# Kernel optimization log

Measured on AMD Instinct MI355X. Metric: run time of the kernel, lower is better.

The kernel has to match this reference:

```python
import jax, jax.numpy as jnp
import numpy as np

D_MODEL = 1024
NHEADS = 16
DIM_K = D_MODEL // NHEADS


def setup_inputs() -> dict:
    key = jax.random.key(0)
    ks = jax.random.split(key, 7)
    B, S = 4, 2048
    scale = 1.0 / np.sqrt(D_MODEL)
    return {
        "Q": jax.random.normal(ks[0], (B, S, D_MODEL), jnp.float32),
        "K": jax.random.normal(ks[1], (B, S, D_MODEL), jnp.float32),
        "V": jax.random.normal(ks[2], (B, S, D_MODEL), jnp.float32),
        "Wq": jax.random.normal(ks[3], (D_MODEL, D_MODEL), jnp.float32) * scale,
        "Wk": jax.random.normal(ks[4], (D_MODEL, D_MODEL), jnp.float32) * scale,
        "Wv": jax.random.normal(ks[5], (D_MODEL, D_MODEL), jnp.float32) * scale,
        "Wo": jax.random.normal(ks[6], (D_MODEL, D_MODEL), jnp.float32) * scale,
    }


def _split(x):
    # [B,S,D] -> [B,H,S,dk]
    B, S, _ = x.shape
    return x.reshape(B, S, NHEADS, DIM_K).transpose(0, 2, 1, 3)


def reference(Q, K, V, Wq, Wk, Wv, Wo):
    # nn.Linear(x) = x @ W.T; weights stored torch-style [out, in]
    q = _split(Q @ Wq.T)  # [B,H,S,dk]
    k = _split(K @ Wk.T)
    v = _split(V @ Wv.T)
    scores = jnp.einsum("bhsd,bhtd->bhst", q, k) / jnp.sqrt(jnp.float32(DIM_K))
    attn = jax.nn.softmax(scores, axis=-1)
    out = jnp.einsum("bhst,bhtd->bhsd", attn, v)  # [B,H,S,dk]
    B, H, S, dk = out.shape
    out = out.transpose(0, 2, 1, 3).reshape(B, S, H * dk)
    return out @ Wo.T
```

## Files before the change

kernel.cpp:

```cpp
#include <hip/hip_runtime.h>
#include <math.h>
#include <stdint.h>

#define D_MODEL 1024
#define NHEADS  16
#define DK      64
#define BATCH   4
#define SEQ     2048
#define MROWS   (BATCH * SEQ)
#define TENS    ((size_t)MROWS * D_MODEL)
#define WELT    ((size_t)D_MODEL * D_MODEL)

typedef __attribute__((ext_vector_type(8))) _Float16 f16x8;
typedef __attribute__((ext_vector_type(2))) __fp16 h16x2;
typedef __attribute__((ext_vector_type(4))) float f32x4;
typedef __attribute__((ext_vector_type(8))) unsigned short us8;
typedef __attribute__((ext_vector_type(4))) unsigned short us4;

__device__ __forceinline__ unsigned short f2h(float x) {
    _Float16 h = (_Float16)x;
    return __builtin_bit_cast(unsigned short, h);
}

#if __has_builtin(__builtin_amdgcn_exp2f)
__device__ __forceinline__ float fexp2(float x) { return __builtin_amdgcn_exp2f(x); }
#else
__device__ __forceinline__ float fexp2(float x) { return exp2f(x); }
#endif

__device__ __forceinline__ void gld_lds16(const void* g, void* l) {
    __builtin_amdgcn_global_load_lds(
        (__attribute__((address_space(1))) void*)(uintptr_t)(g),
        (__attribute__((address_space(3))) void*)(unsigned)(uintptr_t)(l),
        16, 0, 0);
}

__global__ __launch_bounds__(256)
void convert_kernel(const float* __restrict__ q, const float* __restrict__ k,
                    const float* __restrict__ v, const float* __restrict__ wq,
                    const float* __restrict__ wk, const float* __restrict__ wv,
                    const float* __restrict__ wo, unsigned short* __restrict__ dst)
{
    const int seg = blockIdx.y;
    const float* src;
    size_t n, doff;
    if (seg < 3) {
        src = (seg == 0) ? q : (seg == 1) ? k : v;
        n = TENS; doff = (size_t)seg * TENS;
    } else {
        src = (seg == 3) ? wq : (seg == 4) ? wk : (seg == 5) ? wv : wo;
        n = WELT; doff = 3 * TENS + (size_t)(seg - 3) * WELT;
    }
    size_t i = ((size_t)blockIdx.x * 256 + threadIdx.x) * 4;
    if (i >= n) return;
    float4 f = *(const float4*)(src + i);
    us4 o = { f2h(f.x), f2h(f.y), f2h(f.z), f2h(f.w) };
    *(us4*)(dst + doff + i) = o;
}

__device__ __forceinline__
void gemm_body(const unsigned short* __restrict__ A,
               const unsigned short* __restrict__ B,
               void* __restrict__ C, int N, int K, int omode,
               unsigned short* As, unsigned short* Bs)
{
    const int tid  = threadIdx.x;
    const int wave = tid >> 6;
    const int lane = tid & 63;
    const int g    = lane >> 4;
    const int m15  = lane & 15;
    const int bm   = blockIdx.x * 128;
    const int bn   = blockIdx.y * 128;

    const int srw = lane >> 3;
    const int lc  = (lane & 7) ^ srw;

    const int wr = (wave >> 1) * 64;
    const int wc = (wave & 1) * 64;

    f32x4 acc[4][4];
#pragma unroll
    for (int i = 0; i < 4; ++i)
#pragma unroll
        for (int j = 0; j < 4; ++j) acc[i][j] = (f32x4){0.f, 0.f, 0.f, 0.f};

    for (int k0 = 0; k0 < K; k0 += 64) {
        __syncthreads();
#pragma unroll
        for (int i = 0; i < 4; ++i) {
            const int rb = wave * 32 + i * 8;
            gld_lds16(A + (size_t)(bm + rb + srw) * K + k0 + lc * 8,
                      &As[rb * 64]);
            gld_lds16(B + (size_t)(bn + rb + srw) * K + k0 + lc * 8,
                      &Bs[rb * 64]);
        }
        __syncthreads();

#pragma unroll
        for (int t = 0; t < 2; ++t) {
            f16x8 af[4], bf[4];
#pragma unroll
            for (int i = 0; i < 4; ++i) {
                int row = wr + i * 16 + m15;
                int pc  = (4 * t + g) ^ (row & 7);
                af[i] = *(const f16x8*)&As[row * 64 + pc * 8];
            }
#pragma unroll
            for (int j = 0; j < 4; ++j) {
                int row = wc + j * 16 + m15;
                int pc  = (4 * t + g) ^ (row & 7);
                bf[j] = *(const f16x8*)&Bs[row * 64 + pc * 8];
            }
#pragma unroll
            for (int i = 0; i < 4; ++i)
#pragma unroll
                for (int j = 0; j < 4; ++j)
                    acc[i][j] = __builtin_amdgcn_mfma_f32_16x16x32_f16(
                        af[i], bf[j], acc[i][j], 0, 0, 0);
        }
    }

#pragma unroll
    for (int i = 0; i < 4; ++i) {
        const int gm0 = bm + wr + i * 16 + g * 4;
#pragma unroll
        for (int j = 0; j < 4; ++j) {
            const int gn = bn + wc + j * 16 + m15;
            if (omode == 0) {
#pragma unroll
                for (int r = 0; r < 4; ++r)
                    ((float*)C)[(size_t)(gm0 + r) * N + gn] = acc[i][j][r];
            } else if (omode == 1) {
#pragma unroll
                for (int r = 0; r < 4; ++r)
                    ((unsigned short*)C)[(size_t)(gm0 + r) * N + gn] = f2h(acc[i][j][r]);
            } else {
                const int b_ = gm0 >> 11, s_ = gm0 & 2047;
                const int h_ = gn >> 6,  d_ = gn & 63;
                us4 o = { f2h(acc[i][j][0]), f2h(acc[i][j][1]),
                          f2h(acc[i][j][2]), f2h(acc[i][j][3]) };
                *(us4*)((unsigned short*)C +
                        (((size_t)(b_ * NHEADS + h_) * DK + d_) << 11) + s_) = o;
            }
        }
    }
}

__global__ __launch_bounds__(256)
void proj3_kernel(const unsigned short* __restrict__ qb,
                  const unsigned short* __restrict__ kb,
                  const unsigned short* __restrict__ vb,
                  const unsigned short* __restrict__ wq,
                  const unsigned short* __restrict__ wk,
                  const unsigned short* __restrict__ wv,
                  unsigned short* __restrict__ qproj,
                  unsigned short* __restrict__ kproj,
                  unsigned short* __restrict__ vtw)
{
    __shared__ unsigned short As[128 * 64];
    __shared__ unsigned short Bs[128 * 64];
    const int z = blockIdx.z;
    const unsigned short* A = (z == 0) ? qb : (z == 1) ? kb : vb;
    const unsigned short* B = (z == 0) ? wq : (z == 1) ? wk : wv;
    void* C = (z == 0) ? (void*)qproj : (z == 1) ? (void*)kproj : (void*)vtw;
    gemm_body(A, B, C, D_MODEL, D_MODEL, (z == 2) ? 2 : 1, As, Bs);
}

__global__ __launch_bounds__(256)
void gemm_out_kernel(const unsigned short* __restrict__ A,
                     const unsigned short* __restrict__ B,
                     float* __restrict__ C)
{
    __shared__ unsigned short As[128 * 64];
    __shared__ unsigned short Bs[128 * 64];
    gemm_body(A, B, C, D_MODEL, D_MODEL, 0, As, Bs);
}

__global__ __launch_bounds__(256, 2)
void attn_kernel(const unsigned short* __restrict__ qp,
                 const unsigned short* __restrict__ kp,
                 const unsigned short* __restrict__ vt,
                 unsigned short* __restrict__ ao)
{
    __shared__ unsigned short Ks[64 * 64];
    __shared__ unsigned short VTs[64 * 64];
    __shared__ unsigned short Ps[4][64 * 72];

    const int tid = threadIdx.x;
    const int w = tid >> 6, lane = tid & 63;
    const int g = lane >> 4, m15 = lane & 15;
    const int qt = blockIdx.x, h = blockIdx.y, b = blockIdx.z;

    const int q0 = qt * 256 + w * 64;
    const size_t rowbase = (size_t)b * SEQ;

    const int srw = lane >> 3;
    const int lc  = (lane & 7) ^ srw;

    const _Float16 qscale = (_Float16)(0.125f * 1.4426950408889634f);
    f16x8 qf[4][2];
#pragma unroll
    for (int mi = 0; mi < 4; ++mi)
#pragma unroll
        for (int t = 0; t < 2; ++t) {
            f16x8 v = *(const f16x8*)(qp + (rowbase + q0 + mi * 16 + m15) * D_MODEL
                                      + h * DK + t * 32 + g * 8);
            qf[mi][t] = v * qscale;
        }

    float mrun[4] = {-INFINITY, -INFINITY, -INFINITY, -INFINITY};
    float lrun[4] = {0.f, 0.f, 0.f, 0.f};

    f32x4 accO[4][4];
#pragma unroll
    for (int mi = 0; mi < 4; ++mi)
#pragma unroll
        for (int i = 0; i < 4; ++i) accO[mi][i] = (f32x4){0.f, 0.f, 0.f, 0.f};

    const unsigned short* kbase = kp + rowbase * D_MODEL + h * DK;
    const unsigned short* vbase = vt + (size_t)(b * NHEADS + h) * DK * SEQ;

    for (int kt = 0; kt < SEQ / 64; ++kt) {
        __syncthreads();
#pragma unroll
        for (int it = 0; it < 2; ++it) {
            const int rb = w * 16 + it * 8;
            gld_lds16(kbase + (size_t)(kt * 64 + rb + srw) * D_MODEL + lc * 8,
                      &Ks[rb * 64]);
            gld_lds16(vbase + (size_t)(rb + srw) * SEQ + kt * 64 + lc * 8,
                      &VTs[rb * 64]);
        }
        __syncthreads();

        f32x4 ST[4][4];
#pragma unroll
        for (int km = 0; km < 4; ++km) {
            const int row = km * 16 + m15;
            f16x8 kf0 = *(const f16x8*)&Ks[row * 64 + ((0 + g) ^ (row & 7)) * 8];
            f16x8 kf1 = *(const f16x8*)&Ks[row * 64 + ((4 + g) ^ (row & 7)) * 8];
#pragma unroll
            for (int mi = 0; mi < 4; ++mi) {
                f32x4 z = (f32x4){0.f, 0.f, 0.f, 0.f};
                z = __builtin_amdgcn_mfma_f32_16x16x32_f16(kf0, qf[mi][0], z, 0, 0, 0);
                z = __builtin_amdgcn_mfma_f32_16x16x32_f16(kf1, qf[mi][1], z, 0, 0, 0);
                ST[km][mi] = z;
            }
        }

        float scl[4];
#pragma unroll
        for (int mi = 0; mi < 4; ++mi) {
            float mx = -INFINITY;
#pragma unroll
            for (int km = 0; km < 4; ++km)
#pragma unroll
                for (int r = 0; r < 4; ++r) mx = fmaxf(mx, ST[km][mi][r]);
            mx = fmaxf(mx, __shfl_xor(mx, 16));
            mx = fmaxf(mx, __shfl_xor(mx, 32));
            float mnew = fmaxf(mrun[mi], mx);
            scl[mi] = fexp2(mrun[mi] - mnew);
            mrun[mi] = mnew;
            float rs = 0.f;
#pragma unroll
            for (int km = 0; km < 4; ++km) {
                float p0 = fexp2(ST[km][mi][0] - mnew);
                float p1 = fexp2(ST[km][mi][1] - mnew);
                float p2 = fexp2(ST[km][mi][2] - mnew);
                float p3 = fexp2(ST[km][mi][3] - mnew);
                rs += (p0 + p1) + (p2 + p3);
                h16x2 d0 = __builtin_amdgcn_cvt_pkrtz(p0, p1);
                h16x2 d1 = __builtin_amdgcn_cvt_pkrtz(p2, p3);
                uint2 wv = { __builtin_bit_cast(unsigned, d0),
                             __builtin_bit_cast(unsigned, d1) };
                *(uint2*)&Ps[w][(mi * 16 + m15) * 72 + km * 16 + g * 4] = wv;
            }
            rs += __shfl_xor(rs, 16);
            rs += __shfl_xor(rs, 32);
            lrun[mi] = lrun[mi] * scl[mi] + rs;
        }

        int chg = (scl[0] < 1.f) | (scl[1] < 1.f) | (scl[2] < 1.f) | (scl[3] < 1.f);
        if (__any(chg)) {
#pragma unroll
            for (int mi = 0; mi < 4; ++mi)
#pragma unroll
                for (int i = 0; i < 4; ++i) accO[mi][i] *= scl[mi];
        }

        f16x8 pf[4][2];
#pragma unroll
        for (int mi = 0; mi < 4; ++mi) {
            pf[mi][0] = *(const f16x8*)&Ps[w][(mi * 16 + m15) * 72 + g * 8];
            pf[mi][1] = *(const f16x8*)&Ps[w][(mi * 16 + m15) * 72 + 32 + g * 8];
        }

#pragma unroll
        for (int i = 0; i < 4; ++i) {
            const int row = i * 16 + m15;
            f16x8 vf0 = *(const f16x8*)&VTs[row * 64 + ((0 + g) ^ (row & 7)) * 8];
            f16x8 vf1 = *(const f16x8*)&VTs[row * 64 + ((4 + g) ^ (row & 7)) * 8];
#pragma unroll
            for (int mi = 0; mi < 4; ++mi) {
                f32x4 a = accO[mi][i];
                a = __builtin_amdgcn_mfma_f32_16x16x32_f16(vf0, pf[mi][0], a, 0, 0, 0);
                a = __builtin_amdgcn_mfma_f32_16x16x32_f16(vf1, pf[mi][1], a, 0, 0, 0);
                accO[mi][i] = a;
            }
        }
    }

#pragma unroll
    for (int mi = 0; mi < 4; ++mi) {
        const float li = 1.f / lrun[mi];
        const size_t qg = rowbase + q0 + mi * 16 + m15;
#pragma unroll
        for (int i = 0; i < 4; ++i) {
            us4 o = { f2h(accO[mi][i][0] * li), f2h(accO[mi][i][1] * li),
                      f2h(accO[mi][i][2] * li), f2h(accO[mi][i][3] * li) };
            *(us4*)(ao + qg * D_MODEL + h * DK + i * 16 + g * 4) = o;
        }
    }
}

extern "C" void kernel_launch(void* const* d_in, const int* in_sizes, int n_in,
                              void* d_out, int out_size, void* d_ws, size_t ws_size,
                              hipStream_t stream)
{
    const float* Q  = (const float*)d_in[0];
    const float* K  = (const float*)d_in[1];
    const float* V  = (const float*)d_in[2];
    const float* Wq = (const float*)d_in[3];
    const float* Wk = (const float*)d_in[4];
    const float* Wv = (const float*)d_in[5];
    const float* Wo = (const float*)d_in[6];

    unsigned short* base = (unsigned short*)d_ws;
    unsigned short* qb = base;
    unsigned short* kb = qb + TENS;
    unsigned short* vb = kb + TENS;
    unsigned short* wq = vb + TENS;
    unsigned short* wk = wq + WELT;
    unsigned short* wv = wk + WELT;
    unsigned short* wo = wv + WELT;
    unsigned short* qproj = wo + WELT;
    unsigned short* kproj = qproj + TENS;
    unsigned short* vtw   = kproj + TENS;
    unsigned short* aow   = vtw + TENS;

    convert_kernel<<<dim3(TENS / 1024, 7), 256, 0, stream>>>(Q, K, V, Wq, Wk, Wv, Wo, base);

    proj3_kernel<<<dim3(MROWS / 128, D_MODEL / 128, 3), 256, 0, stream>>>(
        qb, kb, vb, wq, wk, wv, qproj, kproj, vtw);

    attn_kernel<<<dim3(SEQ / 256, NHEADS, BATCH), 256, 0, stream>>>(
        qproj, kproj, vtw, aow);

    gemm_out_kernel<<<dim3(MROWS / 128, D_MODEL / 128), 256, 0, stream>>>(
        aow, wo, (float*)d_out);
}
```

Before: 346.3 us.

## Halve attention query tile per wave, raise occupancy, swizzle P buffer, merge weight conversion

The attention kernel now gives each wave 32 query rows instead of 64 and each block 128 rows, so the grid doubles and launch bounds ask for 4 blocks per CU. The P staging buffer drops its padding in favour of an XOR swizzle, and the MFMA sections are wrapped in s_setprio. The convert kernel packs the four weight matrices into one grid segment, which removes the many idle blocks the weight segments used to launch. The trade-off is more K/V tile loads per query row in exchange for higher occupancy and better latency hiding.

New measurement: 358.5 us. +3.5%, slower.

```diff
diff --git a/kernel.cpp b/kernel.cpp
--- a/kernel.cpp
+++ b/kernel.cpp
@@ -42,20 +42,24 @@
                     const float* __restrict__ wo, unsigned short* __restrict__ dst)
 {
     const int seg = blockIdx.y;
+    size_t i = ((size_t)blockIdx.x * 256 + threadIdx.x) * 4;
     const float* src;
-    size_t n, doff;
+    size_t doff, soff;
     if (seg < 3) {
+        if (i >= TENS) return;
         src = (seg == 0) ? q : (seg == 1) ? k : v;
-        n = TENS; doff = (size_t)seg * TENS;
+        soff = i;
+        doff = (size_t)seg * TENS + i;
     } else {
-        src = (seg == 3) ? wq : (seg == 4) ? wk : (seg == 5) ? wv : wo;
-        n = WELT; doff = 3 * TENS + (size_t)(seg - 3) * WELT;
-    }
-    size_t i = ((size_t)blockIdx.x * 256 + threadIdx.x) * 4;
-    if (i >= n) return;
-    float4 f = *(const float4*)(src + i);
+        if (i >= 4 * WELT) return;
+        const int widx = (int)(i >> 20);
+        src = (widx == 0) ? wq : (widx == 1) ? wk : (widx == 2) ? wv : wo;
+        soff = i & (WELT - 1);
+        doff = 3 * TENS + i;
+    }
+    float4 f = *(const float4*)(src + soff);
     us4 o = { f2h(f.x), f2h(f.y), f2h(f.z), f2h(f.w) };
-    *(us4*)(dst + doff + i) = o;
+    *(us4*)(dst + doff) = o;
 }
 
 __device__ __forceinline__
@@ -176,7 +180,7 @@
     gemm_body(A, B, C, D_MODEL, D_MODEL, 0, As, Bs);
 }
 
-__global__ __launch_bounds__(256, 2)
+__global__ __launch_bounds__(256, 4)
 void attn_kernel(const unsigned short* __restrict__ qp,
                  const unsigned short* __restrict__ kp,
                  const unsigned short* __restrict__ vt,
@@ -184,23 +188,23 @@
 {
     __shared__ unsigned short Ks[64 * 64];
     __shared__ unsigned short VTs[64 * 64];
-    __shared__ unsigned short Ps[4][64 * 72];
+    __shared__ unsigned short Ps[4][32 * 64];
 
     const int tid = threadIdx.x;
     const int w = tid >> 6, lane = tid & 63;
     const int g = lane >> 4, m15 = lane & 15;
     const int qt = blockIdx.x, h = blockIdx.y, b = blockIdx.z;
 
-    const int q0 = qt * 256 + w * 64;
+    const int q0 = qt * 128 + w * 32;
     const size_t rowbase = (size_t)b * SEQ;
 
     const int srw = lane >> 3;
     const int lc  = (lane & 7) ^ srw;
 
     const _Float16 qscale = (_Float16)(0.125f * 1.4426950408889634f);
-    f16x8 qf[4][2];
-#pragma unroll
-    for (int mi = 0; mi < 4; ++mi)
+    f16x8 qf[2][2];
+#pragma unroll
+    for (int mi = 0; mi < 2; ++mi)
 #pragma unroll
         for (int t = 0; t < 2; ++t) {
             f16x8 v = *(const f16x8*)(qp + (rowbase + q0 + mi * 16 + m15) * D_MODEL
@@ -208,12 +212,12 @@
             qf[mi][t] = v * qscale;
         }
 
-    float mrun[4] = {-INFINITY, -INFINITY, -INFINITY, -INFINITY};
-    float lrun[4] = {0.f, 0.f, 0.f, 0.f};
-
-    f32x4 accO[4][4];
-#pragma unroll
-    for (int mi = 0; mi < 4; ++mi)
+    float mrun[2] = {-INFINITY, -INFINITY};
+    float lrun[2] = {0.f, 0.f};
+
+    f32x4 accO[2][4];
+#pragma unroll
+    for (int mi = 0; mi < 2; ++mi)
 #pragma unroll
         for (int i = 0; i < 4; ++i) accO[mi][i] = (f32x4){0.f, 0.f, 0.f, 0.f};
 
@@ -232,24 +236,27 @@
         }
         __syncthreads();
 
-        f32x4 ST[4][4];
+        f32x4 ST[4][2];
+        __builtin_amdgcn_s_setprio(1);
 #pragma unroll
         for (int km = 0; km < 4; ++km) {
             const int row = km * 16 + m15;
             f16x8 kf0 = *(const f16x8*)&Ks[row * 64 + ((0 + g) ^ (row & 7)) * 8];
             f16x8 kf1 = *(const f16x8*)&Ks[row * 64 + ((4 + g) ^ (row & 7)) * 8];
 #pragma unroll
-            for (int mi = 0; mi < 4; ++mi) {
+            for (int mi = 0; mi < 2; ++mi) {
                 f32x4 z = (f32x4){0.f, 0.f, 0.f, 0.f};
                 z = __builtin_amdgcn_mfma_f32_16x16x32_f16(kf0, qf[mi][0], z, 0, 0, 0);
                 z = __builtin_amdgcn_mfma_f32_16x16x32_f16(kf1, qf[mi][1], z, 0, 0, 0);
                 ST[km][mi] = z;
             }
         }
-
-        float scl[4];
-#pragma unroll
-        for (int mi = 0; mi < 4; ++mi) {
+        __builtin_amdgcn_s_setprio(0);
+
+        float scl[2];
+#pragma unroll
+        for (int mi = 0; mi < 2; ++mi) {
+            const int prow = mi * 16 + m15;
             float mx = -INFINITY;
 #pragma unroll
             for (int km = 0; km < 4; ++km)
@@ -272,45 +279,49 @@
                 h16x2 d1 = __builtin_amdgcn_cvt_pkrtz(p2, p3);
                 uint2 wv = { __builtin_bit_cast(unsigned, d0),
                              __builtin_bit_cast(unsigned, d1) };
-                *(uint2*)&Ps[w][(mi * 16 + m15) * 72 + km * 16 + g * 4] = wv;
+                const int pc = (km * 2 + (g >> 1)) ^ (prow & 7);
+                *(uint2*)&Ps[w][prow * 64 + pc * 8 + (g & 1) * 4] = wv;
             }
             rs += __shfl_xor(rs, 16);
             rs += __shfl_xor(rs, 32);
             lrun[mi] = lrun[mi] * scl[mi] + rs;
         }
 
-        int chg = (scl[0] < 1.f) | (scl[1] < 1.f) | (scl[2] < 1.f) | (scl[3] < 1.f);
+        int chg = (scl[0] < 1.f) | (scl[1] < 1.f);
         if (__any(chg)) {
 #pragma unroll
-            for (int mi = 0; mi < 4; ++mi)
+            for (int mi = 0; mi < 2; ++mi)
 #pragma unroll
                 for (int i = 0; i < 4; ++i) accO[mi][i] *= scl[mi];
         }
 
-        f16x8 pf[4][2];
-#pragma unroll
-        for (int mi = 0; mi < 4; ++mi) {
-            pf[mi][0] = *(const f16x8*)&Ps[w][(mi * 16 + m15) * 72 + g * 8];
-            pf[mi][1] = *(const f16x8*)&Ps[w][(mi * 16 + m15) * 72 + 32 + g * 8];
-        }
-
+        f16x8 pf[2][2];
+#pragma unroll
+        for (int mi = 0; mi < 2; ++mi) {
+            const int prow = mi * 16 + m15;
+            pf[mi][0] = *(const f16x8*)&Ps[w][prow * 64 + ((0 + g) ^ (prow & 7)) * 8];
+            pf[mi][1] = *(const f16x8*)&Ps[w][prow * 64 + ((4 + g) ^ (prow & 7)) * 8];
+        }
+
+        __builtin_amdgcn_s_setprio(1);
 #pragma unroll
         for (int i = 0; i < 4; ++i) {
             const int row = i * 16 + m15;
             f16x8 vf0 = *(const f16x8*)&VTs[row * 64 + ((0 + g) ^ (row & 7)) * 8];
             f16x8 vf1 = *(const f16x8*)&VTs[row * 64 + ((4 + g) ^ (row & 7)) * 8];
 #pragma unroll
-            for (int mi = 0; mi < 4; ++mi) {
+            for (int mi = 0; mi < 2; ++mi) {
                 f32x4 a = accO[mi][i];
                 a = __builtin_amdgcn_mfma_f32_16x16x32_f16(vf0, pf[mi][0], a, 0, 0, 0);
                 a = __builtin_amdgcn_mfma_f32_16x16x32_f16(vf1, pf[mi][1], a, 0, 0, 0);
                 accO[mi][i] = a;
             }
         }
-    }
-
-#pragma unroll
-    for (int mi = 0; mi < 4; ++mi) {
+        __builtin_amdgcn_s_setprio(0);
+    }
+
+#pragma unroll
+    for (int mi = 0; mi < 2; ++mi) {
         const float li = 1.f / lrun[mi];
         const size_t qg = rowbase + q0 + mi * 16 + m15;
 #pragma unroll
@@ -347,12 +358,12 @@
     unsigned short* vtw   = kproj + TENS;
     unsigned short* aow   = vtw + TENS;
 
-    convert_kernel<<<dim3(TENS / 1024, 7), 256, 0, stream>>>(Q, K, V, Wq, Wk, Wv, Wo, base);
+    convert_kernel<<<dim3(TENS / 1024, 4), 256, 0, stream>>>(Q, K, V, Wq, Wk, Wv, Wo, base);
 
     proj3_kernel<<<dim3(MROWS / 128, D_MODEL / 128, 3), 256, 0, stream>>>(
         qb, kb, vb, wq, wk, wv, qproj, kproj, vtw);
 
-    attn_kernel<<<dim3(SEQ / 256, NHEADS, BATCH), 256, 0, stream>>>(
+    attn_kernel<<<dim3(SEQ / 128, NHEADS, BATCH), 256, 0, stream>>>(
         qproj, kproj, vtw, aow);
 
     gemm_out_kernel<<<dim3(MROWS / 128, D_MODEL / 128), 256, 0, stream>>>(
```

## Double-buffer K/V tiles in attention and merge weight conversion segments

Applied to the files above, without the earlier changes.

The attention kernel now double-buffers the K and V^T LDS tiles, so the next tile is loaded while the current one is computed, with a single barrier per iteration. The P scratch buffer is cut to one 16-row slice per wave, reused for each mi row block. s_setprio is raised around the MFMA sections. The convert kernel folds the four weight matrices into a single grid segment, dropping three mostly-empty grid rows. The trade-offs are more LDS for K/V (offset by the smaller P buffer) and the loss of overlap between the P writes and reads for different mi blocks.

Result: no change. 346.5 us (+0.0%).

```diff
diff --git a/kernel.cpp b/kernel.cpp
--- a/kernel.cpp
+++ b/kernel.cpp
@@ -42,20 +42,24 @@
                     const float* __restrict__ wo, unsigned short* __restrict__ dst)
 {
     const int seg = blockIdx.y;
+    size_t i = ((size_t)blockIdx.x * 256 + threadIdx.x) * 4;
     const float* src;
-    size_t n, doff;
+    size_t doff, soff;
     if (seg < 3) {
+        if (i >= TENS) return;
         src = (seg == 0) ? q : (seg == 1) ? k : v;
-        n = TENS; doff = (size_t)seg * TENS;
+        soff = i;
+        doff = (size_t)seg * TENS + i;
     } else {
-        src = (seg == 3) ? wq : (seg == 4) ? wk : (seg == 5) ? wv : wo;
-        n = WELT; doff = 3 * TENS + (size_t)(seg - 3) * WELT;
-    }
-    size_t i = ((size_t)blockIdx.x * 256 + threadIdx.x) * 4;
-    if (i >= n) return;
-    float4 f = *(const float4*)(src + i);
+        if (i >= 4 * WELT) return;
+        const int widx = (int)(i >> 20);
+        src = (widx == 0) ? wq : (widx == 1) ? wk : (widx == 2) ? wv : wo;
+        soff = i & (WELT - 1);
+        doff = 3 * TENS + i;
+    }
+    float4 f = *(const float4*)(src + soff);
     us4 o = { f2h(f.x), f2h(f.y), f2h(f.z), f2h(f.w) };
-    *(us4*)(dst + doff + i) = o;
+    *(us4*)(dst + doff) = o;
 }
 
 __device__ __forceinline__
@@ -182,9 +186,9 @@
                  const unsigned short* __restrict__ vt,
                  unsigned short* __restrict__ ao)
 {
-    __shared__ unsigned short Ks[64 * 64];
-    __shared__ unsigned short VTs[64 * 64];
-    __shared__ unsigned short Ps[4][64 * 72];
+    __shared__ unsigned short Ks[2][64 * 64];
+    __shared__ unsigned short VTs[2][64 * 64];
+    __shared__ unsigned short Ps[4][16 * 72];
 
     const int tid = threadIdx.x;
     const int w = tid >> 6, lane = tid & 63;
@@ -220,24 +224,32 @@
     const unsigned short* kbase = kp + rowbase * D_MODEL + h * DK;
     const unsigned short* vbase = vt + (size_t)(b * NHEADS + h) * DK * SEQ;
 
-    for (int kt = 0; kt < SEQ / 64; ++kt) {
-        __syncthreads();
+    auto stage = [&](int buf, int t) {
 #pragma unroll
         for (int it = 0; it < 2; ++it) {
             const int rb = w * 16 + it * 8;
-            gld_lds16(kbase + (size_t)(kt * 64 + rb + srw) * D_MODEL + lc * 8,
-                      &Ks[rb * 64]);
-            gld_lds16(vbase + (size_t)(rb + srw) * SEQ + kt * 64 + lc * 8,
-                      &VTs[rb * 64]);
-        }
-        __syncthreads();
+            gld_lds16(kbase + (size_t)(t * 64 + rb + srw) * D_MODEL + lc * 8,
+                      &Ks[buf][rb * 64]);
+            gld_lds16(vbase + (size_t)(rb + srw) * SEQ + t * 64 + lc * 8,
+                      &VTs[buf][rb * 64]);
+        }
+    };
+
+    const int NT = SEQ / 64;
+    stage(0, 0);
+    __syncthreads();
+
+    for (int kt = 0; kt < NT; ++kt) {
+        const int cur = kt & 1;
+        if (kt + 1 < NT) stage(cur ^ 1, kt + 1);
 
         f32x4 ST[4][4];
+        __builtin_amdgcn_s_setprio(1);
 #pragma unroll
         for (int km = 0; km < 4; ++km) {
             const int row = km * 16 + m15;
-            f16x8 kf0 = *(const f16x8*)&Ks[row * 64 + ((0 + g) ^ (row & 7)) * 8];
-            f16x8 kf1 = *(const f16x8*)&Ks[row * 64 + ((4 + g) ^ (row & 7)) * 8];
+            f16x8 kf0 = *(const f16x8*)&Ks[cur][row * 64 + ((0 + g) ^ (row & 7)) * 8];
+            f16x8 kf1 = *(const f16x8*)&Ks[cur][row * 64 + ((4 + g) ^ (row & 7)) * 8];
 #pragma unroll
             for (int mi = 0; mi < 4; ++mi) {
                 f32x4 z = (f32x4){0.f, 0.f, 0.f, 0.f};
@@ -246,8 +258,10 @@
                 ST[km][mi] = z;
             }
         }
+        __builtin_amdgcn_s_setprio(0);
 
         float scl[4];
+        f16x8 pf[4][2];
 #pragma unroll
         for (int mi = 0; mi < 4; ++mi) {
             float mx = -INFINITY;
@@ -272,11 +286,13 @@
                 h16x2 d1 = __builtin_amdgcn_cvt_pkrtz(p2, p3);
                 uint2 wv = { __builtin_bit_cast(unsigned, d0),
                              __builtin_bit_cast(unsigned, d1) };
-                *(uint2*)&Ps[w][(mi * 16 + m15) * 72 + km * 16 + g * 4] = wv;
+                *(uint2*)&Ps[w][m15 * 72 + km * 16 + g * 4] = wv;
             }
             rs += __shfl_xor(rs, 16);
             rs += __shfl_xor(rs, 32);
             lrun[mi] = lrun[mi] * scl[mi] + rs;
+            pf[mi][0] = *(const f16x8*)&Ps[w][m15 * 72 + g * 8];
+            pf[mi][1] = *(const f16x8*)&Ps[w][m15 * 72 + 32 + g * 8];
         }
 
         int chg = (scl[0] < 1.f) | (scl[1] < 1.f) | (scl[2] < 1.f) | (scl[3] < 1.f);
@@ -287,18 +303,12 @@
                 for (int i = 0; i < 4; ++i) accO[mi][i] *= scl[mi];
         }
 
-        f16x8 pf[4][2];
-#pragma unroll
-        for (int mi = 0; mi < 4; ++mi) {
-            pf[mi][0] = *(const f16x8*)&Ps[w][(mi * 16 + m15) * 72 + g * 8];
-            pf[mi][1] = *(const f16x8*)&Ps[w][(mi * 16 + m15) * 72 + 32 + g * 8];
-        }
-
+        __builtin_amdgcn_s_setprio(1);
 #pragma unroll
         for (int i = 0; i < 4; ++i) {
             const int row = i * 16 + m15;
-            f16x8 vf0 = *(const f16x8*)&VTs[row * 64 + ((0 + g) ^ (row & 7)) * 8];
-            f16x8 vf1 = *(const f16x8*)&VTs[row * 64 + ((4 + g) ^ (row & 7)) * 8];
+            f16x8 vf0 = *(const f16x8*)&VTs[cur][row * 64 + ((0 + g) ^ (row & 7)) * 8];
+            f16x8 vf1 = *(const f16x8*)&VTs[cur][row * 64 + ((4 + g) ^ (row & 7)) * 8];
 #pragma unroll
             for (int mi = 0; mi < 4; ++mi) {
                 f32x4 a = accO[mi][i];
@@ -307,6 +317,9 @@
                 accO[mi][i] = a;
             }
         }
+        __builtin_amdgcn_s_setprio(0);
+
+        __syncthreads();
     }
 
 #pragma unroll
@@ -347,7 +360,7 @@
     unsigned short* vtw   = kproj + TENS;
     unsigned short* aow   = vtw + TENS;
 
-    convert_kernel<<<dim3(TENS / 1024, 7), 256, 0, stream>>>(Q, K, V, Wq, Wk, Wv, Wo, base);
+    convert_kernel<<<dim3(TENS / 1024, 4), 256, 0, stream>>>(Q, K, V, Wq, Wk, Wv, Wo, base);
 
     proj3_kernel<<<dim3(MROWS / 128, D_MODEL / 128, 3), 256, 0, stream>>>(
         qb, kb, vb, wq, wk, wv, qproj, kproj, vtw);
```
